# Performance work log

Measured on AMD Instinct MI355X. Metric: run time of the kernel, lower is better.

Reference implementation:

```python
import jax, jax.numpy as jnp
import numpy as np

V, E, H, B, T, K = 50000, 100, 128, 128, 512, 12
HD = H // 2  # per-direction LSTM hidden = 64
START, STOP = 10, 11


def _lstm_params(k):
    k1, k2, k3, k4 = jax.random.split(k, 4)
    s = 1.0 / np.sqrt(HD)
    return (jax.random.uniform(k1, (4 * HD, E), minval=-s, maxval=s),
            jax.random.uniform(k2, (4 * HD, HD), minval=-s, maxval=s),
            jax.random.uniform(k3, (4 * HD,), minval=-s, maxval=s),
            jax.random.uniform(k4, (4 * HD,), minval=-s, maxval=s))


def setup_inputs() -> dict:
    key = jax.random.key(0)
    ks = jax.random.split(key, 10)
    sentences = jax.random.randint(ks[0], (B, T), 0, V)
    emb = jax.random.normal(ks[1], (V, E)) * 0.1
    Wih_f, Whh_f, bih_f, bhh_f = _lstm_params(ks[2])
    Wih_b, Whh_b, bih_b, bhh_b = _lstm_params(ks[3])
    W_out = jax.random.normal(ks[4], (K, H)) * 0.05
    b_out = jnp.zeros((K,), dtype=jnp.float32)
    transitions = jax.random.normal(ks[5], (K, K))
    transitions = transitions.at[:, START].set(-10000.0).at[STOP, :].set(-10000.0)
    h0 = jax.random.normal(ks[6], (2, B, HD))
    c0 = jax.random.normal(ks[7], (2, B, HD))
    return dict(sentences=sentences, emb=emb,
                Wih_f=Wih_f, Whh_f=Whh_f, bih_f=bih_f, bhh_f=bhh_f,
                Wih_b=Wih_b, Whh_b=Whh_b, bih_b=bih_b, bhh_b=bhh_b,
                W_out=W_out, b_out=b_out, transitions=transitions, h0=h0, c0=c0)


def _lstm_dir(x, h0, c0, Wih, Whh, bih, bhh):
    # x: [T,B,E]; PyTorch gate order i,f,g,o
    def step(carry, xt):
        h, c = carry
        g = xt @ Wih.T + h @ Whh.T + bih + bhh  # [B,4HD]
        i, f, gg, o = jnp.split(g, 4, axis=-1)
        c = jax.nn.sigmoid(f) * c + jax.nn.sigmoid(i) * jnp.tanh(gg)
        h = jax.nn.sigmoid(o) * jnp.tanh(c)
        return (h, c), h
    _, hs = jax.lax.scan(step, (h0, c0), x)
    return hs  # [T,B,HD]


def _viterbi(emis, trans):
    # emis: [T,K]
    def step(prev, em_t):
        v = prev[:, None] + trans          # [K_from, K_to]
        nxt = em_t + jnp.max(v, axis=0)
        return nxt, jnp.argmax(v, axis=0)  # backpointer per to-tag
    last, bps = jax.lax.scan(step, emis[0], emis[1:])  # bps: [T-1,K]
    last_tag = jnp.argmax(last)
    score = jnp.max(last)
    def back(tag, bp):
        prev = bp[tag]
        return prev, prev
    _, head = jax.lax.scan(back, last_tag, bps, reverse=True)  # tags[0..T-2]
    path = jnp.concatenate([head, last_tag[None]])
    return score, path


def reference(sentences, emb, Wih_f, Whh_f, bih_f, bhh_f,
              Wih_b, Whh_b, bih_b, bhh_b, W_out, b_out,
              transitions, h0, c0):
    x = emb[sentences]              # [B,T,E]
    xt = jnp.swapaxes(x, 0, 1)      # [T,B,E]
    hf = _lstm_dir(xt, h0[0], c0[0], Wih_f, Whh_f, bih_f, bhh_f)
    hb = _lstm_dir(xt[::-1], h0[1], c0[1], Wih_b, Whh_b, bih_b, bhh_b)[::-1]
    hcat = jnp.concatenate([hf, hb], axis=-1)      # [T,B,H]
    emis = hcat @ W_out.T + b_out                  # [T,B,K]
    emis = jnp.swapaxes(emis, 0, 1)                # [B,T,K]
    scores, paths = jax.vmap(lambda e: _viterbi(e, transitions))(emis)
    return scores, paths
```

## Files before the change

### kernel.cpp

```cpp
#include <hip/hip_runtime.h>
#include <hip/hip_bf16.h>

#define VV 50000
#define EE 100
#define HD 64
#define BB 128
#define TT 512
#define KK 12

typedef unsigned int uint32;
typedef __bf16 bf16x8 __attribute__((ext_vector_type(8)));
typedef float  f32x4  __attribute__((ext_vector_type(4)));

__device__ __forceinline__ float bf_lo(unsigned u) { return __uint_as_float(u << 16); }
__device__ __forceinline__ float bf_hi(unsigned u) { return __uint_as_float(u & 0xffff0000u); }
__device__ __forceinline__ float rl_f(float v, int lane) {
    return __uint_as_float(__builtin_amdgcn_readlane(__float_as_uint(v), lane));
}
__device__ __forceinline__ float sigm_f(float x) { return 1.f / (1.f + __expf(-x)); }
__device__ __forceinline__ float tanh_f(float x) {
    float e = __expf(2.f * x);
    return 1.f - 2.f / (e + 1.f);
}
__device__ __forceinline__ unsigned short f2bf(float v) {
    return __builtin_bit_cast(unsigned short, __float2bfloat16(v));
}
__device__ __forceinline__ void lds_barrier() {
    asm volatile("s_waitcnt lgkmcnt(0)" ::: "memory");
    __builtin_amdgcn_s_barrier();
    asm volatile("" ::: "memory");
}

#define LDK 136

__global__ __launch_bounds__(256) void k1_mfma(
    const float* __restrict__ emb,
    const float* __restrict__ Wih_f, const float* __restrict__ Wih_b,
    __hip_bfloat16* __restrict__ proj)
{
    __shared__ unsigned short lA[64 * LDK];
    __shared__ unsigned short lB[64 * LDK];

    const int tid = threadIdx.x;
    const int v0  = blockIdx.x * 64;

    for (int i = tid; i < 64 * 20; i += 256) {
        int r = i / 20, c2 = i % 20;
        *(uint32*)&lA[r * LDK + 96 + c2 * 2] = 0u;
        *(uint32*)&lB[r * LDK + 96 + c2 * 2] = 0u;
    }
    {
        const float* asrc = emb + (size_t)v0 * EE;
        const int alim = (VV - v0 < 64 ? VV - v0 : 64) * EE;
        for (int i = tid; i < 64 * EE; i += 256) {
            float v = (i < alim) ? asrc[i] : 0.f;
            lA[(i / EE) * LDK + (i % EE)] = f2bf(v);
        }
    }
    __syncthreads();

    const int w = tid >> 6, l = tid & 63;
    const int lo16 = l & 15, hi = l >> 4;

    bf16x8 afr[4];
    #pragma unroll
    for (int s = 0; s < 4; ++s)
        afr[s] = *(const bf16x8*)&lA[(w * 16 + lo16) * LDK + s * 32 + hi * 8];

    for (int jb = 0; jb < 8; ++jb) {
        const float* Wsrc = ((jb < 4) ? Wih_f : Wih_b) + (size_t)(jb & 3) * 64 * EE;
        __syncthreads();
        for (int i = tid; i < 64 * EE; i += 256)
            lB[(i / EE) * LDK + (i % EE)] = f2bf(Wsrc[i]);
        __syncthreads();

        f32x4 acc[4] = { {0.f,0.f,0.f,0.f}, {0.f,0.f,0.f,0.f},
                         {0.f,0.f,0.f,0.f}, {0.f,0.f,0.f,0.f} };
        #pragma unroll
        for (int s = 0; s < 4; ++s) {
            #pragma unroll
            for (int n = 0; n < 4; ++n) {
                bf16x8 bfr = *(const bf16x8*)&lB[(n * 16 + lo16) * LDK + s * 32 + hi * 8];
                acc[n] = __builtin_amdgcn_mfma_f32_16x16x32_bf16(afr[s], bfr, acc[n], 0, 0, 0);
            }
        }
        #pragma unroll
        for (int n = 0; n < 4; ++n) {
            #pragma unroll
            for (int r = 0; r < 4; ++r) {
                int v = v0 + w * 16 + hi * 4 + r;
                int j = jb * 64 + n * 16 + lo16;
                if (v < VV)
                    proj[(size_t)v * 512 + j] = __float2bfloat16(acc[n][r]);
            }
        }
    }
}

__global__ __launch_bounds__(256, 2) void k2_lstm(
    const int* __restrict__ sent,
    const __hip_bfloat16* __restrict__ proj,
    const float* __restrict__ Whh_f, const float* __restrict__ Whh_b,
    const float* __restrict__ bih_f, const float* __restrict__ bhh_f,
    const float* __restrict__ bih_b, const float* __restrict__ bhh_b,
    const float* __restrict__ h0, const float* __restrict__ c0,
    __hip_bfloat16* __restrict__ Hbuf)
{
    const int b   = blockIdx.x >> 1;
    const int d   = blockIdx.x & 1;
    const int tid = threadIdx.x;
    const int u   = tid & 63;
    const int w   = tid >> 6;

    __shared__ float a_lds[2][256];

    const float* Whh = (d == 0 ? Whh_f : Whh_b) + (size_t)tid * HD;
    float wreg[HD];
    #pragma unroll
    for (int k = 0; k < HD / 4; ++k) {
        float4 t = reinterpret_cast<const float4*>(Whh)[k];
        wreg[4*k+0] = t.x; wreg[4*k+1] = t.y; wreg[4*k+2] = t.z; wreg[4*k+3] = t.w;
    }
    const float bias = (d == 0) ? (bih_f[tid] + bhh_f[tid]) : (bih_b[tid] + bhh_b[tid]);

    float h = h0[((size_t)d * BB + b) * HD + u];
    float c = c0[((size_t)d * BB + b) * HD + u];

    const int* srow = sent + (size_t)b * TT;
    const int tstep = (d == 0) ? 1 : -1;
    const int t0    = (d == 0) ? 0 : TT - 1;
    const int doff  = d * 256;
    const unsigned short* prj = (const unsigned short*)proj;

    uint32 cur[8], nxt[8];
    #pragma unroll
    for (int i = 0; i < 8; ++i)
        cur[i] = prj[(size_t)srow[t0 + i * tstep] * 512 + doff + tid];

    __hip_bfloat16* hp = Hbuf + ((size_t)t0 * BB + b) * 128 + d * 64 + u;
    const ptrdiff_t hstride = (ptrdiff_t)tstep * BB * 128;

    int pb = 0;
    for (int s0 = 0; s0 < TT; s0 += 8) {
        #pragma unroll
        for (int i = 0; i < 8; ++i) {
            int sn = s0 + 8 + i;
            sn = (sn < TT) ? sn : TT - 1;
            nxt[i] = prj[(size_t)srow[t0 + sn * tstep] * 512 + doff + tid];
        }
        #pragma unroll
        for (int i = 0; i < 8; ++i) {
            const float xp = bf_lo(cur[i]);

            float acc0 = bias + xp, acc1 = 0.f, acc2 = 0.f, acc3 = 0.f;
            #pragma unroll
            for (int k = 0; k < HD; k += 4) {
                float hk0 = rl_f(h, k + 0);
                float hk1 = rl_f(h, k + 1);
                float hk2 = rl_f(h, k + 2);
                float hk3 = rl_f(h, k + 3);
                acc0 = fmaf(hk0, wreg[k + 0], acc0);
                acc1 = fmaf(hk1, wreg[k + 1], acc1);
                acc2 = fmaf(hk2, wreg[k + 2], acc2);
                acc3 = fmaf(hk3, wreg[k + 3], acc3);
            }
            float g = (acc0 + acc1) + (acc2 + acc3);

            float a = (w == 2) ? tanh_f(g) : sigm_f(g);
            a_lds[pb][tid] = a;
            lds_barrier();
            float ai = a_lds[pb][u];
            float af = a_lds[pb][64 + u];
            float ag = a_lds[pb][128 + u];
            float ao = a_lds[pb][192 + u];
            c = af * c + ai * ag;
            h = ao * tanh_f(c);
            pb ^= 1;

            if (tid < 64)
                *hp = __float2bfloat16(h);
            hp += hstride;
        }
        #pragma unroll
        for (int i = 0; i < 8; ++i) cur[i] = nxt[i];
    }
}

__global__ __launch_bounds__(128) void k3_emis(
    const __hip_bfloat16* __restrict__ Hbuf,
    const float* __restrict__ W_out, const float* __restrict__ b_out,
    float* __restrict__ emis)
{
    const int t = blockIdx.x;
    const int b = threadIdx.x;
    __shared__ float Wl[KK * 128];
    for (int i = threadIdx.x; i < KK * 128; i += 128) Wl[i] = W_out[i];
    __syncthreads();

    const __hip_bfloat16* hrow = Hbuf + ((size_t)t * BB + b) * 128;
    float acc[KK];
    #pragma unroll
    for (int k = 0; k < KK; ++k) acc[k] = b_out[k];

    #pragma unroll
    for (int u0 = 0; u0 < 128; u0 += 8) {
        uint4 hv = *reinterpret_cast<const uint4*>(hrow + u0);
        float hf[8];
        hf[0] = bf_lo(hv.x); hf[1] = bf_hi(hv.x);
        hf[2] = bf_lo(hv.y); hf[3] = bf_hi(hv.y);
        hf[4] = bf_lo(hv.z); hf[5] = bf_hi(hv.z);
        hf[6] = bf_lo(hv.w); hf[7] = bf_hi(hv.w);
        #pragma unroll
        for (int k = 0; k < KK; ++k) {
            #pragma unroll
            for (int r = 0; r < 8; ++r)
                acc[k] = fmaf(hf[r], Wl[k * 128 + u0 + r], acc[k]);
        }
    }
    float* e = emis + ((size_t)b * TT + t) * KK;
    #pragma unroll
    for (int k = 0; k < KK; k += 4) {
        float4 v = make_float4(acc[k], acc[k+1], acc[k+2], acc[k+3]);
        *reinterpret_cast<float4*>(e + k) = v;
    }
}

__global__ __launch_bounds__(64) void k4_viterbi(
    const float* __restrict__ emis, const float* __restrict__ trans,
    float* __restrict__ out)
{
    const int b    = blockIdx.x;
    const int lane = threadIdx.x;
    __shared__ float em_lds[TT * KK];
    __shared__ unsigned char bp[(TT - 1) * KK + 4];

    {
        const uint4* e4 = reinterpret_cast<const uint4*>(emis + (size_t)b * TT * KK);
        uint4* l4 = reinterpret_cast<uint4*>(em_lds);
        for (int i = lane; i < TT * KK / 4; i += 64) l4[i] = e4[i];
    }
    __syncthreads();

    const int jj = (lane < KK) ? lane : 0;
    float tc[KK];
    #pragma unroll
    for (int i = 0; i < KK; ++i) tc[i] = trans[i * KK + jj];

    float vj = em_lds[jj];
    float sv[KK];
    #pragma unroll
    for (int i = 0; i < KK; ++i) sv[i] = rl_f(vj, i);

    for (int t = 1; t < TT; ++t) {
        float best = sv[0] + tc[0];
        int bi = 0;
        #pragma unroll
        for (int i = 1; i < KK; ++i) {
            float cnd = sv[i] + tc[i];
            bool gt = cnd > best;
            best = gt ? cnd : best;
            bi   = gt ? i : bi;
        }
        if (lane < KK) bp[(t - 1) * KK + lane] = (unsigned char)bi;
        vj = best + em_lds[t * KK + jj];
        #pragma unroll
        for (int i = 0; i < KK; ++i) sv[i] = rl_f(vj, i);
    }

    float best = sv[0]; int bt = 0;
    #pragma unroll
    for (int i = 1; i < KK; ++i) { if (sv[i] > best) { best = sv[i]; bt = i; } }

    if (lane == 0) {
        out[b] = best;
        float* path = out + BB + (size_t)b * TT;
        int tag = bt;
        path[TT - 1] = (float)tag;
        for (int t = TT - 2; t >= 0; --t) {
            tag = bp[t * KK + tag];
            path[t] = (float)tag;
        }
    }
}

extern "C" void kernel_launch(void* const* d_in, const int* in_sizes, int n_in,
                              void* d_out, int out_size, void* d_ws, size_t ws_size,
                              hipStream_t stream) {
    const int*   sent  = (const int*)  d_in[0];
    const float* emb   = (const float*)d_in[1];
    const float* Wih_f = (const float*)d_in[2];
    const float* Whh_f = (const float*)d_in[3];
    const float* bih_f = (const float*)d_in[4];
    const float* bhh_f = (const float*)d_in[5];
    const float* Wih_b = (const float*)d_in[6];
    const float* Whh_b = (const float*)d_in[7];
    const float* bih_b = (const float*)d_in[8];
    const float* bhh_b = (const float*)d_in[9];
    const float* W_out = (const float*)d_in[10];
    const float* b_out = (const float*)d_in[11];
    const float* trans = (const float*)d_in[12];
    const float* h0    = (const float*)d_in[13];
    const float* c0    = (const float*)d_in[14];
    float* out = (float*)d_out;

    char* ws = (char*)d_ws;
    __hip_bfloat16* proj = (__hip_bfloat16*)ws;
    size_t off = (((size_t)VV * 512 * 2) + 255) & ~(size_t)255;
    __hip_bfloat16* Hbuf = (__hip_bfloat16*)(ws + off);
    off += (((size_t)TT * BB * 128 * 2) + 255) & ~(size_t)255;
    float* emis = (float*)(ws + off);

    k1_mfma<<<dim3((VV + 63) / 64), 256, 0, stream>>>(emb, Wih_f, Wih_b, proj);
    k2_lstm<<<dim3(2 * BB), 256, 0, stream>>>(sent, proj, Whh_f, Whh_b,
                                              bih_f, bhh_f, bih_b, bhh_b,
                                              h0, c0, Hbuf);
    k3_emis<<<dim3(TT), 128, 0, stream>>>(Hbuf, W_out, b_out, emis);
    k4_viterbi<<<dim3(BB), 64, 0, stream>>>(emis, trans, out);
}
```

Before: 540.3 us.

## Run LSTM recurrence in a single wave with packed fp16 dot2 products

The recurrent kernel now uses one 64-lane wave per (batch, direction) instead of four waves. Each lane computes all four gates for its hidden unit, which removes the LDS exchange and the block barrier on every timestep. The recurrent weights are stored in registers as packed fp16 pairs. h is paired via DPP and broadcast with readlane, then consumed with v_dot2 instructions, which halves the broadcasts and FMAs per gate. This risks fp16 precision loss on the weights and hidden state, plus higher register pressure and lower occupancy.

```diff
diff --git a/kernel.cpp b/kernel.cpp
--- a/kernel.cpp
+++ b/kernel.cpp
@@ -11,6 +11,7 @@
 typedef unsigned int uint32;
 typedef __bf16 bf16x8 __attribute__((ext_vector_type(8)));
 typedef float  f32x4  __attribute__((ext_vector_type(4)));
+typedef _Float16 half2v __attribute__((ext_vector_type(2)));
 
 __device__ __forceinline__ float bf_lo(unsigned u) { return __uint_as_float(u << 16); }
 __device__ __forceinline__ float bf_hi(unsigned u) { return __uint_as_float(u & 0xffff0000u); }
@@ -25,10 +26,12 @@
 __device__ __forceinline__ unsigned short f2bf(float v) {
     return __builtin_bit_cast(unsigned short, __float2bfloat16(v));
 }
-__device__ __forceinline__ void lds_barrier() {
-    asm volatile("s_waitcnt lgkmcnt(0)" ::: "memory");
-    __builtin_amdgcn_s_barrier();
-    asm volatile("" ::: "memory");
+__device__ __forceinline__ float fdot2(half2v a, half2v b, float c) {
+#if __has_builtin(__builtin_amdgcn_fdot2)
+    return __builtin_amdgcn_fdot2(a, b, c, false);
+#else
+    return c + (float)a[0] * (float)b[0] + (float)a[1] * (float)b[1];
+#endif
 }
 
 #define LDK 136
@@ -97,7 +100,7 @@
     }
 }
 
-__global__ __launch_bounds__(256, 2) void k2_lstm(
+__global__ __launch_bounds__(64, 1) void k2_lstm(
     const int* __restrict__ sent,
     const __hip_bfloat16* __restrict__ proj,
     const float* __restrict__ Whh_f, const float* __restrict__ Whh_b,
@@ -106,22 +109,29 @@
     const float* __restrict__ h0, const float* __restrict__ c0,
     __hip_bfloat16* __restrict__ Hbuf)
 {
-    const int b   = blockIdx.x >> 1;
-    const int d   = blockIdx.x & 1;
-    const int tid = threadIdx.x;
-    const int u   = tid & 63;
-    const int w   = tid >> 6;
-
-    __shared__ float a_lds[2][256];
-
-    const float* Whh = (d == 0 ? Whh_f : Whh_b) + (size_t)tid * HD;
-    float wreg[HD];
-    #pragma unroll
-    for (int k = 0; k < HD / 4; ++k) {
-        float4 t = reinterpret_cast<const float4*>(Whh)[k];
-        wreg[4*k+0] = t.x; wreg[4*k+1] = t.y; wreg[4*k+2] = t.z; wreg[4*k+3] = t.w;
-    }
-    const float bias = (d == 0) ? (bih_f[tid] + bhh_f[tid]) : (bih_b[tid] + bhh_b[tid]);
+    const int b = blockIdx.x >> 1;
+    const int d = blockIdx.x & 1;
+    const int u = threadIdx.x;
+
+    const float* Wbase = (d == 0) ? Whh_f : Whh_b;
+    const float* bihp  = (d == 0) ? bih_f : bih_b;
+    const float* bhhp  = (d == 0) ? bhh_f : bhh_b;
+
+    half2v wpk[4][32];
+    #pragma unroll
+    for (int g = 0; g < 4; ++g) {
+        const float* row = Wbase + (size_t)(g * 64 + u) * HD;
+        #pragma unroll
+        for (int p = 0; p < 16; ++p) {
+            float4 w4 = reinterpret_cast<const float4*>(row)[p];
+            wpk[g][2*p]   = half2v{(_Float16)w4.x, (_Float16)w4.y};
+            wpk[g][2*p+1] = half2v{(_Float16)w4.z, (_Float16)w4.w};
+        }
+    }
+    float bias[4];
+    #pragma unroll
+    for (int g = 0; g < 4; ++g)
+        bias[g] = bihp[g * 64 + u] + bhhp[g * 64 + u];
 
     float h = h0[((size_t)d * BB + b) * HD + u];
     float c = c0[((size_t)d * BB + b) * HD + u];
@@ -132,57 +142,62 @@
     const int doff  = d * 256;
     const unsigned short* prj = (const unsigned short*)proj;
 
-    uint32 cur[8], nxt[8];
-    #pragma unroll
-    for (int i = 0; i < 8; ++i)
-        cur[i] = prj[(size_t)srow[t0 + i * tstep] * 512 + doff + tid];
+    uint32 cur[4][4], nxt[4][4];
+    #pragma unroll
+    for (int i = 0; i < 4; ++i) {
+        size_t base = (size_t)srow[t0 + i * tstep] * 512 + doff + u;
+        #pragma unroll
+        for (int g = 0; g < 4; ++g) cur[i][g] = prj[base + g * 64];
+    }
 
     __hip_bfloat16* hp = Hbuf + ((size_t)t0 * BB + b) * 128 + d * 64 + u;
     const ptrdiff_t hstride = (ptrdiff_t)tstep * BB * 128;
 
-    int pb = 0;
-    for (int s0 = 0; s0 < TT; s0 += 8) {
-        #pragma unroll
-        for (int i = 0; i < 8; ++i) {
-            int sn = s0 + 8 + i;
+    for (int s0 = 0; s0 < TT; s0 += 4) {
+        #pragma unroll
+        for (int i = 0; i < 4; ++i) {
+            int sn = s0 + 4 + i;
             sn = (sn < TT) ? sn : TT - 1;
-            nxt[i] = prj[(size_t)srow[t0 + sn * tstep] * 512 + doff + tid];
-        }
-        #pragma unroll
-        for (int i = 0; i < 8; ++i) {
-            const float xp = bf_lo(cur[i]);
-
-            float acc0 = bias + xp, acc1 = 0.f, acc2 = 0.f, acc3 = 0.f;
-            #pragma unroll
-            for (int k = 0; k < HD; k += 4) {
-                float hk0 = rl_f(h, k + 0);
-                float hk1 = rl_f(h, k + 1);
-                float hk2 = rl_f(h, k + 2);
-                float hk3 = rl_f(h, k + 3);
-                acc0 = fmaf(hk0, wreg[k + 0], acc0);
-                acc1 = fmaf(hk1, wreg[k + 1], acc1);
-                acc2 = fmaf(hk2, wreg[k + 2], acc2);
-                acc3 = fmaf(hk3, wreg[k + 3], acc3);
+            size_t base = (size_t)srow[t0 + sn * tstep] * 512 + doff + u;
+            #pragma unroll
+            for (int g = 0; g < 4; ++g) nxt[i][g] = prj[base + g * 64];
+        }
+        #pragma unroll
+        for (int i = 0; i < 4; ++i) {
+            int hpart = __builtin_amdgcn_update_dpp(
+                0, __float_as_int(h), 0xB1, 0xF, 0xF, false);
+            half2v hp2 = __builtin_bit_cast(half2v,
+                __builtin_amdgcn_cvt_pkrtz(h, __int_as_float(hpart)));
+            uint32 hbits = __builtin_bit_cast(uint32, hp2);
+
+            float a0 = bias[0] + bf_lo(cur[i][0]);
+            float a1 = bias[1] + bf_lo(cur[i][1]);
+            float a2 = bias[2] + bf_lo(cur[i][2]);
+            float a3 = bias[3] + bf_lo(cur[i][3]);
+            #pragma unroll
+            for (int p = 0; p < 32; ++p) {
+                uint32 hs = (uint32)__builtin_amdgcn_readlane((int)hbits, 2 * p);
+                half2v hv = __builtin_bit_cast(half2v, hs);
+                a0 = fdot2(wpk[0][p], hv, a0);
+                a1 = fdot2(wpk[1][p], hv, a1);
+                a2 = fdot2(wpk[2][p], hv, a2);
+                a3 = fdot2(wpk[3][p], hv, a3);
             }
-            float g = (acc0 + acc1) + (acc2 + acc3);
-
-            float a = (w == 2) ? tanh_f(g) : sigm_f(g);
-            a_lds[pb][tid] = a;
-            lds_barrier();
-            float ai = a_lds[pb][u];
-            float af = a_lds[pb][64 + u];
-            float ag = a_lds[pb][128 + u];
-            float ao = a_lds[pb][192 + u];
-            c = af * c + ai * ag;
-            h = ao * tanh_f(c);
-            pb ^= 1;
-
-            if (tid < 64)
-                *hp = __float2bfloat16(h);
+            float gi = sigm_f(a0);
+            float gf = sigm_f(a1);
+            float gg = tanh_f(a2);
+            float go = sigm_f(a3);
+            c = gf * c + gi * gg;
+            h = go * tanh_f(c);
+
+            *hp = __float2bfloat16(h);
             hp += hstride;
         }
         #pragma unroll
-        for (int i = 0; i < 8; ++i) cur[i] = nxt[i];
+        for (int i = 0; i < 4; ++i) {
+            #pragma unroll
+            for (int g = 0; g < 4; ++g) cur[i][g] = nxt[i][g];
+        }
     }
 }
 
@@ -311,9 +326,9 @@
     float* emis = (float*)(ws + off);
 
     k1_mfma<<<dim3((VV + 63) / 64), 256, 0, stream>>>(emb, Wih_f, Wih_b, proj);
-    k2_lstm<<<dim3(2 * BB), 256, 0, stream>>>(sent, proj, Whh_f, Whh_b,
-                                              bih_f, bhh_f, bih_b, bhh_b,
-                                              h0, c0, Hbuf);
+    k2_lstm<<<dim3(2 * BB), 64, 0, stream>>>(sent, proj, Whh_f, Whh_b,
+                                             bih_f, bhh_f, bih_b, bhh_b,
+                                             h0, c0, Hbuf);
     k3_emis<<<dim3(TT), 128, 0, stream>>>(Hbuf, W_out, b_out, emis);
     k4_viterbi<<<dim3(BB), 64, 0, stream>>>(emis, trans, out);
 }
```

New measurement: 552.3 us. +2.2%, slower.
